# Kernel tuning notes

Hardware: AMD Instinct MI355X
Metric: run time of the kernel (lower is better)

Reference implementation:

```python
import jax, jax.numpy as jnp
import numpy as np

BATCH, H, NFAM = 32768, 1024, 10


def setup_inputs() -> dict:
    key = jax.random.key(0)
    k1, k2, k3, k4 = jax.random.split(key, 4)
    scale1 = 1.0 / np.sqrt(2 * H)
    scale2 = 1.0 / np.sqrt(H)
    return {
        "features": jax.random.normal(k1, (BATCH, H), dtype=jnp.float32),
        "prototypes": jax.random.normal(k2, (NFAM, H), dtype=jnp.float32),
        "W1": jax.random.normal(k3, (2 * H, H), dtype=jnp.float32) * scale1,
        "b1": jnp.zeros((H,), dtype=jnp.float32),
        "W2": jax.random.normal(k4, (H, H), dtype=jnp.float32) * scale2,
        "b2": jnp.zeros((H,), dtype=jnp.float32),
    }


def reference(features, prototypes, W1, b1, W2, b2):
    # Squared euclidean distances via the norm trick (avoids [B, NFAM, H] blowup).
    # argmin over squared distances == argmin over cdist (sqrt is monotone).
    f2 = jnp.sum(features * features, axis=1, keepdims=True)        # [B, 1]
    p2 = jnp.sum(prototypes * prototypes, axis=1)                   # [NFAM]
    d2 = f2 + p2[None, :] - 2.0 * (features @ prototypes.T)         # [B, NFAM]
    nearest_idx = jnp.argmin(d2, axis=1)                            # [B]
    nearest_prototypes = prototypes[nearest_idx]                    # [B, H]
    combined = jnp.concatenate([features, nearest_prototypes], axis=1)  # [B, 2H]
    hidden = jax.nn.relu(combined @ W1 + b1)                        # [B, H]
    adapted = hidden @ W2 + b2                                      # [B, H]
    return adapted
```

## Files before the change

### kernel.cpp

```cpp
#include <hip/hip_runtime.h>
#include <stdint.h>
#include <stddef.h>

#define BATCH 32768
#define HDIM  1024
#define NFAM  10

typedef short bf16x8 __attribute__((ext_vector_type(8)));
typedef float f32x4  __attribute__((ext_vector_type(4)));

__device__ __forceinline__ unsigned short f2bf(float x) {
  unsigned int u = __builtin_bit_cast(unsigned int, x);
  u += 0x7fffu + ((u >> 16) & 1u);
  return (unsigned short)(u >> 16);
}

__device__ __forceinline__ void async_cp16(unsigned short* lds_dst, const unsigned short* g_src) {
  __builtin_amdgcn_global_load_lds(
      (const __attribute__((address_space(1))) unsigned int*)g_src,
      (__attribute__((address_space(3))) unsigned int*)lds_dst,
      16, 0, 0);
}

__global__ __launch_bounds__(256) void transpose_cast(
    const float* __restrict__ in, unsigned short* __restrict__ out, int R, int C) {
  __shared__ float tile[64][65];
  const int t = threadIdx.x;
  const int c = t & 63;
  const int r0 = t >> 6;
  const int rbase = blockIdx.y * 64, cbase = blockIdx.x * 64;
#pragma unroll
  for (int i = 0; i < 16; ++i) {
    int r = r0 + i * 4;
    tile[r][c] = in[(size_t)(rbase + r) * C + cbase + c];
  }
  __syncthreads();
#pragma unroll
  for (int i = 0; i < 16; ++i) {
    int r = r0 + i * 4;
    out[(size_t)(cbase + r) * R + rbase + c] = f2bf(tile[c][r]);
  }
}

__global__ __launch_bounds__(256) void proto_prep(
    const float* __restrict__ protos, unsigned short* __restrict__ protosB,
    float* __restrict__ p2) {
  __shared__ float red[4];
  const int j = blockIdx.x, t = threadIdx.x;
  float4 v = ((const float4*)(protos + (size_t)j * HDIM))[t];
  uint2 pk;
  pk.x = (unsigned)f2bf(v.x) | ((unsigned)f2bf(v.y) << 16);
  pk.y = (unsigned)f2bf(v.z) | ((unsigned)f2bf(v.w) << 16);
  *(uint2*)(protosB + (size_t)j * HDIM + t * 4) = pk;
  float s = v.x * v.x + v.y * v.y + v.z * v.z + v.w * v.w;
#pragma unroll
  for (int o = 32; o > 0; o >>= 1) s += __shfl_down(s, o);
  if ((t & 63) == 0) red[t >> 6] = s;
  __syncthreads();
  if (t == 0) p2[j] = red[0] + red[1] + red[2] + red[3];
}

__global__ __launch_bounds__(256) void nearest_kernel(
    const float* __restrict__ feats, const float* __restrict__ protos,
    const float* __restrict__ p2, unsigned short* __restrict__ featsB,
    int* __restrict__ idx) {
  __shared__ float pl[NFAM * HDIM];
  const int t = threadIdx.x;
#pragma unroll
  for (int j = 0; j < NFAM; ++j)
    ((float4*)pl)[t + 256 * j] = ((const float4*)protos)[t + 256 * j];
  __syncthreads();

  const int wave = t >> 6, lane = t & 63;
  float P2[NFAM];
#pragma unroll
  for (int j = 0; j < NFAM; ++j) P2[j] = p2[j];

#pragma unroll
  for (int rr = 0; rr < 4; ++rr) {
    const int row = blockIdx.x * 16 + wave * 4 + rr;
    const float* f = feats + (size_t)row * HDIM;

    float dot[NFAM];
#pragma unroll
    for (int j = 0; j < NFAM; ++j) dot[j] = 0.f;
    float f2 = 0.f;

#pragma unroll
    for (int ch = 0; ch < 4; ++ch) {
      const int k4 = ch * 64 + lane;
      float4 v = ((const float4*)f)[k4];
      f2 += v.x * v.x + v.y * v.y + v.z * v.z + v.w * v.w;
#pragma unroll
      for (int j = 0; j < NFAM; ++j) {
        float4 p = ((const float4*)pl)[j * 256 + k4];
        dot[j] += v.x * p.x + v.y * p.y + v.z * p.z + v.w * p.w;
      }
      uint2 pk;
      pk.x = (unsigned)f2bf(v.x) | ((unsigned)f2bf(v.y) << 16);
      pk.y = (unsigned)f2bf(v.z) | ((unsigned)f2bf(v.w) << 16);
      *(uint2*)(featsB + (size_t)row * HDIM + k4 * 4) = pk;
    }

#pragma unroll
    for (int o = 32; o > 0; o >>= 1) {
      f2 += __shfl_down(f2, o);
#pragma unroll
      for (int j = 0; j < NFAM; ++j) dot[j] += __shfl_down(dot[j], o);
    }
    if (lane == 0) {
      int best = 0;
      float bd = f2 + P2[0] - 2.f * dot[0];
#pragma unroll
      for (int j = 1; j < NFAM; ++j) {
        float d = f2 + P2[j] - 2.f * dot[j];
        if (d < bd) { bd = d; best = j; }
      }
      idx[row] = best;
    }
  }
}

template <int K, int GATHER, int RELU_BF16>
__global__ __launch_bounds__(256) void gemm_kernel(
    const unsigned short* __restrict__ A,
    const unsigned short* __restrict__ P,
    const int* __restrict__ idx,
    const unsigned short* __restrict__ Bt,
    const float* __restrict__ bias,
    unsigned short* __restrict__ outB,
    float* __restrict__ outF) {
  __shared__ unsigned short ldsA[2][128 * 32];
  __shared__ unsigned short ldsB[2][128 * 32];
  __shared__ int idxLds[128];

  const int t    = threadIdx.x;
  const int lane = t & 63;
  const int wid  = t >> 6;
  const int quad = lane >> 4;
  const int r16  = lane & 15;

  const int b = blockIdx.x;
  const int rowBase = ((b >> 6) * 8 + (b & 7)) * 128;
  const int colBase = ((b >> 3) & 7) * 128;
  const int wm = (wid >> 1) * 64;
  const int wn = (wid & 1) * 64;

  if (GATHER) {
    if (t < 128) idxLds[t] = idx[rowBase + t];
    __syncthreads();
  }

  f32x4 acc[4][4];
#pragma unroll
  for (int i = 0; i < 4; ++i)
#pragma unroll
    for (int j = 0; j < 4; ++j) acc[i][j] = (f32x4){0.f, 0.f, 0.f, 0.f};

  const int r0 = t >> 2, r1 = r0 + 64;
  const int q = (t & 3) ^ ((t >> 3) & 3);
  const unsigned short* bB0 = Bt + (size_t)(colBase + r0) * K + q * 8;
  const unsigned short* bB1 = Bt + (size_t)(colBase + r1) * K + q * 8;

  const int pr = quad ^ ((r16 >> 1) & 3);

  for (int kb = 0; kb < K; kb += 64) {
    const unsigned short *aBase0, *aBase1;
    int koff;
    if (!GATHER || kb < 1024) {
      aBase0 = A + (size_t)(rowBase + r0) * 1024 + q * 8;
      aBase1 = A + (size_t)(rowBase + r1) * 1024 + q * 8;
      koff = kb;
    } else {
      aBase0 = P + (size_t)idxLds[r0] * 1024 + q * 8;
      aBase1 = P + (size_t)idxLds[r1] * 1024 + q * 8;
      koff = kb - 1024;
    }
#pragma unroll
    for (int s = 0; s < 2; ++s) {
      async_cp16(&ldsA[s][t * 8],         aBase0 + koff + s * 32);
      async_cp16(&ldsA[s][(t + 256) * 8], aBase1 + koff + s * 32);
      async_cp16(&ldsB[s][t * 8],         bB0 + kb + s * 32);
      async_cp16(&ldsB[s][(t + 256) * 8], bB1 + kb + s * 32);
    }
    __syncthreads();

#pragma unroll
    for (int s = 0; s < 2; ++s) {
      bf16x8 af[4], bfr[4];
#pragma unroll
      for (int mi = 0; mi < 4; ++mi)
        af[mi] = *(const bf16x8*)(&ldsA[s][(wm + mi * 16 + r16) * 32 + pr * 8]);
#pragma unroll
      for (int ni = 0; ni < 4; ++ni)
        bfr[ni] = *(const bf16x8*)(&ldsB[s][(wn + ni * 16 + r16) * 32 + pr * 8]);
#pragma unroll
      for (int mi = 0; mi < 4; ++mi)
#pragma unroll
        for (int ni = 0; ni < 4; ++ni)
          acc[mi][ni] = __builtin_amdgcn_mfma_f32_16x16x32_bf16(af[mi], bfr[ni], acc[mi][ni], 0, 0, 0);
    }
    __syncthreads();
  }

#pragma unroll
  for (int mi = 0; mi < 4; ++mi) {
#pragma unroll
    for (int ni = 0; ni < 4; ++ni) {
      const int grow0 = rowBase + wm + mi * 16 + quad * 4;
      const int gcol  = colBase + wn + ni * 16 + r16;
      const float bv = bias[gcol];
#pragma unroll
      for (int r = 0; r < 4; ++r) {
        float v = acc[mi][ni][r] + bv;
        if (RELU_BF16) {
          v = fmaxf(v, 0.0f);
          outB[(size_t)(grow0 + r) * 1024 + gcol] = f2bf(v);
        } else {
          outF[(size_t)(grow0 + r) * 1024 + gcol] = v;
        }
      }
    }
  }
}

extern "C" void kernel_launch(void* const* d_in, const int* in_sizes, int n_in,
                              void* d_out, int out_size, void* d_ws, size_t ws_size,
                              hipStream_t stream) {
  const float* feats  = (const float*)d_in[0];
  const float* protos = (const float*)d_in[1];
  const float* W1     = (const float*)d_in[2];
  const float* b1     = (const float*)d_in[3];
  const float* W2     = (const float*)d_in[4];
  const float* b2     = (const float*)d_in[5];
  float* out = (float*)d_out;

  unsigned short* featsB  = (unsigned short*)d_ws;
  unsigned short* hiddenB = featsB + (size_t)BATCH * HDIM;
  unsigned short* W1t     = hiddenB + (size_t)BATCH * HDIM;
  unsigned short* W2t     = W1t + (size_t)2 * HDIM * HDIM;
  unsigned short* protosB = W2t + (size_t)HDIM * HDIM;
  float* p2 = (float*)(protosB + NFAM * HDIM);
  int* idx  = (int*)(p2 + NFAM + 2);

  transpose_cast<<<dim3(HDIM / 64, 2 * HDIM / 64), 256, 0, stream>>>(W1, W1t, 2 * HDIM, HDIM);
  transpose_cast<<<dim3(HDIM / 64, HDIM / 64), 256, 0, stream>>>(W2, W2t, HDIM, HDIM);
  proto_prep<<<NFAM, 256, 0, stream>>>(protos, protosB, p2);
  nearest_kernel<<<BATCH / 16, 256, 0, stream>>>(feats, protos, p2, featsB, idx);
  gemm_kernel<2048, 1, 1><<<2048, 256, 0, stream>>>(
      featsB, protosB, idx, W1t, b1, hiddenB, nullptr);
  gemm_kernel<1024, 0, 0><<<2048, 256, 0, stream>>>(
      hiddenB, nullptr, nullptr, W2t, b2, nullptr, out);
}
```

Before: 448.2 us.

## Precompute prototype-W1 products and add them in GEMM epilogue instead of K=2048

Splits the first GEMM algebraically: combined@W1 = features@W1_top + protos[idx]@W1_bottom. The second term is precomputed once per prototype (10x1024 table including b1) by a small fp32 kernel and gathered in the epilogue, so the first GEMM shrinks from K=2048 to K=1024. This removes half of the first GEMM's MFMA work and its gathered prototype loads. In exchange it adds scattered per-row table reads in the epilogue, and the prototype half is now computed in fp32 rather than bf16.

```diff
diff --git a/kernel.cpp b/kernel.cpp
--- a/kernel.cpp
+++ b/kernel.cpp
@@ -43,21 +43,34 @@
 }
 
 __global__ __launch_bounds__(256) void proto_prep(
-    const float* __restrict__ protos, unsigned short* __restrict__ protosB,
-    float* __restrict__ p2) {
+    const float* __restrict__ protos, float* __restrict__ p2) {
   __shared__ float red[4];
   const int j = blockIdx.x, t = threadIdx.x;
   float4 v = ((const float4*)(protos + (size_t)j * HDIM))[t];
-  uint2 pk;
-  pk.x = (unsigned)f2bf(v.x) | ((unsigned)f2bf(v.y) << 16);
-  pk.y = (unsigned)f2bf(v.z) | ((unsigned)f2bf(v.w) << 16);
-  *(uint2*)(protosB + (size_t)j * HDIM + t * 4) = pk;
   float s = v.x * v.x + v.y * v.y + v.z * v.z + v.w * v.w;
 #pragma unroll
   for (int o = 32; o > 0; o >>= 1) s += __shfl_down(s, o);
   if ((t & 63) == 0) red[t >> 6] = s;
   __syncthreads();
   if (t == 0) p2[j] = red[0] + red[1] + red[2] + red[3];
+}
+
+__global__ __launch_bounds__(256) void proto_contrib(
+    const float* __restrict__ protos, const float* __restrict__ W1,
+    const float* __restrict__ b1, float* __restrict__ protoC) {
+  const int j = blockIdx.y;
+  const int n = blockIdx.x * 256 + threadIdx.x;
+  const float* w = W1 + (size_t)HDIM * HDIM + n;
+  const float* p = protos + (size_t)j * HDIM;
+  float s0 = 0.f, s1 = 0.f, s2 = 0.f, s3 = 0.f;
+#pragma unroll 4
+  for (int k = 0; k < HDIM; k += 4) {
+    s0 += p[k]     * w[(size_t)k * HDIM];
+    s1 += p[k + 1] * w[(size_t)(k + 1) * HDIM];
+    s2 += p[k + 2] * w[(size_t)(k + 2) * HDIM];
+    s3 += p[k + 3] * w[(size_t)(k + 3) * HDIM];
+  }
+  protoC[j * HDIM + n] = (s0 + s1) + (s2 + s3) + b1[n];
 }
 
 __global__ __launch_bounds__(256) void nearest_kernel(
@@ -121,15 +134,16 @@
   }
 }
 
-template <int K, int GATHER, int RELU_BF16>
+template <int EPI>
 __global__ __launch_bounds__(256) void gemm_kernel(
     const unsigned short* __restrict__ A,
-    const unsigned short* __restrict__ P,
+    const unsigned short* __restrict__ Bt,
     const int* __restrict__ idx,
-    const unsigned short* __restrict__ Bt,
+    const float* __restrict__ protoC,
     const float* __restrict__ bias,
     unsigned short* __restrict__ outB,
     float* __restrict__ outF) {
+  constexpr int K = 1024;
   __shared__ unsigned short ldsA[2][128 * 32];
   __shared__ unsigned short ldsB[2][128 * 32];
   __shared__ int idxLds[128];
@@ -146,7 +160,7 @@
   const int wm = (wid >> 1) * 64;
   const int wn = (wid & 1) * 64;
 
-  if (GATHER) {
+  if (EPI) {
     if (t < 128) idxLds[t] = idx[rowBase + t];
     __syncthreads();
   }
@@ -159,27 +173,18 @@
 
   const int r0 = t >> 2, r1 = r0 + 64;
   const int q = (t & 3) ^ ((t >> 3) & 3);
+  const unsigned short* aBase0 = A + (size_t)(rowBase + r0) * K + q * 8;
+  const unsigned short* aBase1 = A + (size_t)(rowBase + r1) * K + q * 8;
   const unsigned short* bB0 = Bt + (size_t)(colBase + r0) * K + q * 8;
   const unsigned short* bB1 = Bt + (size_t)(colBase + r1) * K + q * 8;
 
   const int pr = quad ^ ((r16 >> 1) & 3);
 
   for (int kb = 0; kb < K; kb += 64) {
-    const unsigned short *aBase0, *aBase1;
-    int koff;
-    if (!GATHER || kb < 1024) {
-      aBase0 = A + (size_t)(rowBase + r0) * 1024 + q * 8;
-      aBase1 = A + (size_t)(rowBase + r1) * 1024 + q * 8;
-      koff = kb;
-    } else {
-      aBase0 = P + (size_t)idxLds[r0] * 1024 + q * 8;
-      aBase1 = P + (size_t)idxLds[r1] * 1024 + q * 8;
-      koff = kb - 1024;
-    }
 #pragma unroll
     for (int s = 0; s < 2; ++s) {
-      async_cp16(&ldsA[s][t * 8],         aBase0 + koff + s * 32);
-      async_cp16(&ldsA[s][(t + 256) * 8], aBase1 + koff + s * 32);
+      async_cp16(&ldsA[s][t * 8],         aBase0 + kb + s * 32);
+      async_cp16(&ldsA[s][(t + 256) * 8], aBase1 + kb + s * 32);
       async_cp16(&ldsB[s][t * 8],         bB0 + kb + s * 32);
       async_cp16(&ldsB[s][(t + 256) * 8], bB1 + kb + s * 32);
     }
@@ -205,20 +210,28 @@
 
 #pragma unroll
   for (int mi = 0; mi < 4; ++mi) {
+    const int lrow0 = wm + mi * 16 + quad * 4;
+    int pid[4];
+    if (EPI) {
+#pragma unroll
+      for (int r = 0; r < 4; ++r) pid[r] = idxLds[lrow0 + r];
+    }
 #pragma unroll
     for (int ni = 0; ni < 4; ++ni) {
-      const int grow0 = rowBase + wm + mi * 16 + quad * 4;
+      const int grow0 = rowBase + lrow0;
       const int gcol  = colBase + wn + ni * 16 + r16;
-      const float bv = bias[gcol];
-#pragma unroll
-      for (int r = 0; r < 4; ++r) {
-        float v = acc[mi][ni][r] + bv;
-        if (RELU_BF16) {
+      if (EPI) {
+#pragma unroll
+        for (int r = 0; r < 4; ++r) {
+          float v = acc[mi][ni][r] + protoC[(size_t)pid[r] * HDIM + gcol];
           v = fmaxf(v, 0.0f);
           outB[(size_t)(grow0 + r) * 1024 + gcol] = f2bf(v);
-        } else {
-          outF[(size_t)(grow0 + r) * 1024 + gcol] = v;
         }
+      } else {
+        const float bv = bias[gcol];
+#pragma unroll
+        for (int r = 0; r < 4; ++r)
+          outF[(size_t)(grow0 + r) * 1024 + gcol] = acc[mi][ni][r] + bv;
       }
     }
   }
@@ -238,17 +251,16 @@
   unsigned short* featsB  = (unsigned short*)d_ws;
   unsigned short* hiddenB = featsB + (size_t)BATCH * HDIM;
   unsigned short* W1t     = hiddenB + (size_t)BATCH * HDIM;
-  unsigned short* W2t     = W1t + (size_t)2 * HDIM * HDIM;
-  unsigned short* protosB = W2t + (size_t)HDIM * HDIM;
-  float* p2 = (float*)(protosB + NFAM * HDIM);
-  int* idx  = (int*)(p2 + NFAM + 2);
-
-  transpose_cast<<<dim3(HDIM / 64, 2 * HDIM / 64), 256, 0, stream>>>(W1, W1t, 2 * HDIM, HDIM);
+  unsigned short* W2t     = W1t + (size_t)HDIM * HDIM;
+  float* protoC = (float*)(W2t + (size_t)HDIM * HDIM);
+  float* p2     = protoC + NFAM * HDIM;
+  int* idx      = (int*)(p2 + NFAM + 2);
+
+  transpose_cast<<<dim3(HDIM / 64, HDIM / 64), 256, 0, stream>>>(W1, W1t, HDIM, HDIM);
   transpose_cast<<<dim3(HDIM / 64, HDIM / 64), 256, 0, stream>>>(W2, W2t, HDIM, HDIM);
-  proto_prep<<<NFAM, 256, 0, stream>>>(protos, protosB, p2);
+  proto_prep<<<NFAM, 256, 0, stream>>>(protos, p2);
+  proto_contrib<<<dim3(HDIM / 256, NFAM), 256, 0, stream>>>(protos, W1, b1, protoC);
   nearest_kernel<<<BATCH / 16, 256, 0, stream>>>(feats, protos, p2, featsB, idx);
-  gemm_kernel<2048, 1, 1><<<2048, 256, 0, stream>>>(
-      featsB, protosB, idx, W1t, b1, hiddenB, nullptr);
-  gemm_kernel<1024, 0, 0><<<2048, 256, 0, stream>>>(
-      hiddenB, nullptr, nullptr, W2t, b2, nullptr, out);
-}
+  gemm_kernel<1><<<2048, 256, 0, stream>>>(featsB, W1t, idx, protoC, nullptr, hiddenB, nullptr);
+  gemm_kernel<0><<<2048, 256, 0, stream>>>(hiddenB, W2t, nullptr, nullptr, b2, nullptr, out);
+}
```

Result: no change. 450.6 us (+0.6%).
